# Kernel optimization log

Measured on AMD Instinct MI355X. Metric: run time of the kernel, lower is better.

The kernel has to match this reference:

```python
import jax, jax.numpy as jnp
import numpy as np


def _piecewise_weights(gt):
    # stats over gt[0,0]; torch.std uses ddof=1
    g00 = gt[0, 0]
    gmin = jnp.min(g00)
    gmean = jnp.mean(g00)
    gmax = jnp.max(g00)
    sd = jnp.std(g00, ddof=1)
    m1 = gmean + sd
    m2 = gmean + 3.0 * sd
    w_low = (gt - gmin) / (m1 - gmin) * 0.2
    w_mid = (gt - m1) / (m2 - m1) * 0.5 + 0.2
    w_high = (gt - m2) / (gmax - m2) * 0.3 + 0.7
    return jnp.where(gt <= m1, w_low, jnp.where(gt <= m2, w_mid, w_high))


def setup_inputs() -> dict:
    key = jax.random.key(0)
    k1, k2 = jax.random.split(key)
    shape = (1, 1, 4096, 4096)
    inputs = jax.random.normal(k1, shape, dtype=jnp.float32)
    targets = jax.random.normal(k2, shape, dtype=jnp.float32)
    return {"inputs": inputs, "targets": targets}


def reference(inputs, targets):
    # gt is a detached clone of targets -> no grad through the weights
    gt = jax.lax.stop_gradient(targets)
    weights = _piecewise_weights(gt)
    loss = jnp.abs(targets - inputs)
    return jnp.mean(loss * weights)
```

## Files before the change

kernel.cpp:

```cpp
#include <hip/hip_runtime.h>
#include <math.h>

#define BS 256
#define NBLK 1024
#define NWAVES (BS / 64)
#define NSLOT 64
#define PER_SLOT (NBLK / NSLOT)
#define FXS 4294967296.0


__device__ inline double wred_sum(double v) {
#pragma unroll
    for (int o = 32; o > 0; o >>= 1) v += __shfl_down(v, o, 64);
    return v;
}
__device__ inline float wred_min(float v) {
#pragma unroll
    for (int o = 32; o > 0; o >>= 1) v = fminf(v, __shfl_down(v, o, 64));
    return v;
}
__device__ inline float wred_max(float v) {
#pragma unroll
    for (int o = 32; o > 0; o >>= 1) v = fmaxf(v, __shfl_down(v, o, 64));
    return v;
}

__device__ inline void acc_stats(float4 v, double& s, double& ss, float& mn, float& mx) {
    mn = fminf(mn, fminf(fminf(v.x, v.y), fminf(v.z, v.w)));
    mx = fmaxf(mx, fmaxf(fmaxf(v.x, v.y), fmaxf(v.z, v.w)));
    s += (double)v.x + (double)v.y + (double)v.z + (double)v.w;
    ss += (double)v.x * v.x + (double)v.y * v.y
        + (double)v.z * v.z + (double)v.w * v.w;
}

__global__ void __launch_bounds__(BS) k_stats(
        const float* __restrict__ t, int n,
        double* __restrict__ bsum, double* __restrict__ bss,
        float* __restrict__ bmn, float* __restrict__ bmx,
        char* __restrict__ slots) {
    if (blockIdx.x == 0) {
        if (threadIdx.x < NSLOT)
            *(long long*)(slots + (size_t)threadIdx.x * 128) = 0ll;
        else if (threadIdx.x < 2 * NSLOT)
            *(unsigned*)(slots + 8192 + (size_t)(threadIdx.x - NSLOT) * 128) = 0u;
    }

    int tid = blockIdx.x * BS + threadIdx.x;
    const int stride = NBLK * BS;
    int n4 = n >> 2;
    const float4* t4 = (const float4*)t;

    double s = 0.0, ss = 0.0;
    float mn = 3.4e38f, mx = -3.4e38f;
    int i = tid;
    for (; i + 3 * stride < n4; i += 4 * stride) {
        float4 a = t4[i];
        float4 b = t4[i + stride];
        float4 c = t4[i + 2 * stride];
        float4 d = t4[i + 3 * stride];
        acc_stats(a, s, ss, mn, mx);
        acc_stats(b, s, ss, mn, mx);
        acc_stats(c, s, ss, mn, mx);
        acc_stats(d, s, ss, mn, mx);
    }
    for (; i < n4; i += stride) {
        float4 a = t4[i];
        acc_stats(a, s, ss, mn, mx);
    }
    if (tid == 0) {
        for (int j = (n4 << 2); j < n; j++) {
            float v = t[j];
            mn = fminf(mn, v); mx = fmaxf(mx, v);
            s += v; ss += (double)v * v;
        }
    }

    s = wred_sum(s); ss = wred_sum(ss); mn = wred_min(mn); mx = wred_max(mx);

    __shared__ double sh_s[NWAVES], sh_ss[NWAVES];
    __shared__ float sh_mn[NWAVES], sh_mx[NWAVES];
    int wid = threadIdx.x >> 6, lane = threadIdx.x & 63;
    if (lane == 0) { sh_s[wid] = s; sh_ss[wid] = ss; sh_mn[wid] = mn; sh_mx[wid] = mx; }
    __syncthreads();
    if (threadIdx.x == 0) {
        double S = sh_s[0], SS = sh_ss[0];
        float MN = sh_mn[0], MX = sh_mx[0];
        for (int k = 1; k < NWAVES; k++) {
            S += sh_s[k]; SS += sh_ss[k];
            MN = fminf(MN, sh_mn[k]); MX = fmaxf(MX, sh_mx[k]);
        }
        bsum[blockIdx.x] = S; bss[blockIdx.x] = SS;
        bmn[blockIdx.x] = MN; bmx[blockIdx.x] = MX;
    }
}

__device__ inline float welem(float g, float x, float gmin, float m1, float m2,
                              float sl, float sm, float shv) {
    float w = (g <= m1) ? (g - gmin) * sl
            : (g <= m2) ? (g - m1) * sm + 0.2f
                        : (g - m2) * shv + 0.7f;
    return fabsf(g - x) * w;
}

__global__ void __launch_bounds__(BS) k_loss(
        const float* __restrict__ x, const float* __restrict__ t, int n,
        const double* __restrict__ sbsum, const double* __restrict__ sbss,
        const float* __restrict__ sbmn, const float* __restrict__ sbmx,
        char* __restrict__ slots, float* __restrict__ out) {
    __shared__ double sh_s[NWAVES], sh_ss[NWAVES];
    __shared__ float sh_mn[NWAVES], sh_mx[NWAVES];
    __shared__ float s_c[8];
    {
        double s = 0.0, ss = 0.0;
        float mn = 3.4e38f, mx = -3.4e38f;
#pragma unroll 4
        for (int i = threadIdx.x; i < NBLK; i += BS) {
            s += sbsum[i]; ss += sbss[i];
            mn = fminf(mn, sbmn[i]); mx = fmaxf(mx, sbmx[i]);
        }
        s = wred_sum(s); ss = wred_sum(ss); mn = wred_min(mn); mx = wred_max(mx);
        int wid = threadIdx.x >> 6, lane = threadIdx.x & 63;
        if (lane == 0) { sh_s[wid] = s; sh_ss[wid] = ss; sh_mn[wid] = mn; sh_mx[wid] = mx; }
        __syncthreads();
        if (threadIdx.x == 0) {
            double S = sh_s[0], SS = sh_ss[0];
            float MN = sh_mn[0], MX = sh_mx[0];
            for (int k = 1; k < NWAVES; k++) {
                S += sh_s[k]; SS += sh_ss[k];
                MN = fminf(MN, sh_mn[k]); MX = fmaxf(MX, sh_mx[k]);
            }
            double dn = (double)n;
            double mean = S / dn;
            double var = (SS - S * S / dn) / (dn - 1.0);
            double sd = sqrt(var);
            float m1 = (float)(mean + sd);
            float m2 = (float)(mean + 3.0 * sd);
            s_c[0] = MN;
            s_c[1] = m1;
            s_c[2] = m2;
            s_c[3] = 0.2f / (m1 - MN);
            s_c[4] = 0.5f / (m2 - m1);
            s_c[5] = 0.3f / (MX - m2);
        }
        __syncthreads();
    }
    float gmin = s_c[0], m1 = s_c[1], m2 = s_c[2];
    float sl = s_c[3], sm = s_c[4], shv = s_c[5];

    int tid = blockIdx.x * BS + threadIdx.x;
    const int stride = NBLK * BS;
    int n4 = n >> 2;
    const float4* x4 = (const float4*)x;
    const float4* t4 = (const float4*)t;

    double acc = 0.0;
    int i = tid;
    for (; i + 3 * stride < n4; i += 4 * stride) {
        float4 t0 = t4[i];
        float4 t1 = t4[i + stride];
        float4 t2 = t4[i + 2 * stride];
        float4 t3 = t4[i + 3 * stride];
        float4 x0 = x4[i];
        float4 x1 = x4[i + stride];
        float4 x2 = x4[i + 2 * stride];
        float4 x3 = x4[i + 3 * stride];
        float e0 = welem(t0.x, x0.x, gmin, m1, m2, sl, sm, shv)
                 + welem(t0.y, x0.y, gmin, m1, m2, sl, sm, shv)
                 + welem(t0.z, x0.z, gmin, m1, m2, sl, sm, shv)
                 + welem(t0.w, x0.w, gmin, m1, m2, sl, sm, shv);
        float e1 = welem(t1.x, x1.x, gmin, m1, m2, sl, sm, shv)
                 + welem(t1.y, x1.y, gmin, m1, m2, sl, sm, shv)
                 + welem(t1.z, x1.z, gmin, m1, m2, sl, sm, shv)
                 + welem(t1.w, x1.w, gmin, m1, m2, sl, sm, shv);
        float e2 = welem(t2.x, x2.x, gmin, m1, m2, sl, sm, shv)
                 + welem(t2.y, x2.y, gmin, m1, m2, sl, sm, shv)
                 + welem(t2.z, x2.z, gmin, m1, m2, sl, sm, shv)
                 + welem(t2.w, x2.w, gmin, m1, m2, sl, sm, shv);
        float e3 = welem(t3.x, x3.x, gmin, m1, m2, sl, sm, shv)
                 + welem(t3.y, x3.y, gmin, m1, m2, sl, sm, shv)
                 + welem(t3.z, x3.z, gmin, m1, m2, sl, sm, shv)
                 + welem(t3.w, x3.w, gmin, m1, m2, sl, sm, shv);
        acc += (double)e0 + (double)e1 + (double)e2 + (double)e3;
    }
    for (; i < n4; i += stride) {
        float4 tv = t4[i], xv = x4[i];
        float e0 = welem(tv.x, xv.x, gmin, m1, m2, sl, sm, shv)
                 + welem(tv.y, xv.y, gmin, m1, m2, sl, sm, shv)
                 + welem(tv.z, xv.z, gmin, m1, m2, sl, sm, shv)
                 + welem(tv.w, xv.w, gmin, m1, m2, sl, sm, shv);
        acc += (double)e0;
    }
    if (tid == 0) {
        for (int j = (n4 << 2); j < n; j++)
            acc += (double)welem(t[j], x[j], gmin, m1, m2, sl, sm, shv);
    }

    acc = wred_sum(acc);
    __shared__ double sh_acc[NWAVES];
    __shared__ int s_fin;
    int wid = threadIdx.x >> 6, lane = threadIdx.x & 63;
    if (lane == 0) sh_acc[wid] = acc;
    __syncthreads();
    if (threadIdx.x == 0) {
        double S = sh_acc[0];
        for (int k = 1; k < NWAVES; k++) S += sh_acc[k];
        int slot = blockIdx.x & (NSLOT - 1);
        long long* lslot = (long long*)(slots + (size_t)slot * 128);
        unsigned*  cslot = (unsigned*)(slots + 8192 + (size_t)slot * 128);
        __hip_atomic_fetch_add(lslot, (long long)llrint(S * FXS),
                               __ATOMIC_RELAXED, __HIP_MEMORY_SCOPE_AGENT);
        asm volatile("s_waitcnt vmcnt(0)" ::: "memory");
        unsigned prev = __hip_atomic_fetch_add(cslot, 1u,
                               __ATOMIC_RELAXED, __HIP_MEMORY_SCOPE_AGENT);
        s_fin = (prev == PER_SLOT - 1) ? 1 : 0;
    }
    __syncthreads();
    if (!s_fin) return;

    if (threadIdx.x < 64) {
        unsigned total;
        do {
            unsigned c = __hip_atomic_load(
                (unsigned*)(slots + 8192 + (size_t)threadIdx.x * 128),
                __ATOMIC_RELAXED, __HIP_MEMORY_SCOPE_AGENT);
#pragma unroll
            for (int o = 32; o > 0; o >>= 1) c += __shfl_down(c, o, 64);
            total = __shfl(c, 0, 64);
            if (total != NBLK) __builtin_amdgcn_s_sleep(32);
        } while (total != NBLK);
        long long v = __hip_atomic_load(
            (long long*)(slots + (size_t)threadIdx.x * 128),
            __ATOMIC_RELAXED, __HIP_MEMORY_SCOPE_AGENT);
#pragma unroll
        for (int o = 32; o > 0; o >>= 1) v += __shfl_down(v, o, 64);
        if (threadIdx.x == 0)
            out[0] = (float)(((double)v / FXS) / (double)n);
    }
}

extern "C" void kernel_launch(void* const* d_in, const int* in_sizes, int n_in,
                              void* d_out, int out_size, void* d_ws, size_t ws_size,
                              hipStream_t stream) {
    const float* inp = (const float*)d_in[0];
    const float* tgt = (const float*)d_in[1];
    int n = in_sizes[0];

    char* ws = (char*)d_ws;
    double* bsum = (double*)(ws);
    double* bss  = (double*)(ws + 8192);
    float*  bmn  = (float*)(ws + 16384);
    float*  bmx  = (float*)(ws + 20480);
    char*   slots = ws + 24576;

    k_stats<<<NBLK, BS, 0, stream>>>(tgt, n, bsum, bss, bmn, bmx, slots);
    k_loss<<<NBLK, BS, 0, stream>>>(inp, tgt, n, bsum, bss, bmn, bmx,
                                    slots, (float*)d_out);
}
```

Baseline: 46.95 us.

## Switch to contiguous per-block chunks with 2048 blocks and branchless weight select

Doubles the grid to 2048 blocks and replaces the grid-stride loop with a contiguous chunk per block, so each block streams one local region of both tensors. The piecewise weight is now computed for all three branches with fma and then selected, which removes divergent branches, and the finalization and workspace layout are adjusted to the larger block count. The cost is more partial results and atomics to combine and a longer partial-stat reduction at the start of every loss block.

```diff
diff --git a/kernel.cpp b/kernel.cpp
--- a/kernel.cpp
+++ b/kernel.cpp
@@ -2,10 +2,10 @@
 #include <math.h>
 
 #define BS 256
-#define NBLK 1024
+#define NB 2048
 #define NWAVES (BS / 64)
 #define NSLOT 64
-#define PER_SLOT (NBLK / NSLOT)
+#define PER_SLOT (NB / NSLOT)
 #define FXS 4294967296.0
 
 
@@ -45,29 +45,30 @@
             *(unsigned*)(slots + 8192 + (size_t)(threadIdx.x - NSLOT) * 128) = 0u;
     }
 
-    int tid = blockIdx.x * BS + threadIdx.x;
-    const int stride = NBLK * BS;
     int n4 = n >> 2;
+    int cpb = (n4 + NB - 1) / NB;
+    int start = blockIdx.x * cpb;
+    int end = min(start + cpb, n4);
     const float4* t4 = (const float4*)t;
 
     double s = 0.0, ss = 0.0;
     float mn = 3.4e38f, mx = -3.4e38f;
-    int i = tid;
-    for (; i + 3 * stride < n4; i += 4 * stride) {
+    int i = start + threadIdx.x;
+    for (; i + 3 * BS < end; i += 4 * BS) {
         float4 a = t4[i];
-        float4 b = t4[i + stride];
-        float4 c = t4[i + 2 * stride];
-        float4 d = t4[i + 3 * stride];
+        float4 b = t4[i + BS];
+        float4 c = t4[i + 2 * BS];
+        float4 d = t4[i + 3 * BS];
         acc_stats(a, s, ss, mn, mx);
         acc_stats(b, s, ss, mn, mx);
         acc_stats(c, s, ss, mn, mx);
         acc_stats(d, s, ss, mn, mx);
     }
-    for (; i < n4; i += stride) {
+    for (; i < end; i += BS) {
         float4 a = t4[i];
         acc_stats(a, s, ss, mn, mx);
     }
-    if (tid == 0) {
+    if (blockIdx.x == 0 && threadIdx.x == 0) {
         for (int j = (n4 << 2); j < n; j++) {
             float v = t[j];
             mn = fminf(mn, v); mx = fmaxf(mx, v);
@@ -96,10 +97,20 @@
 
 __device__ inline float welem(float g, float x, float gmin, float m1, float m2,
                               float sl, float sm, float shv) {
-    float w = (g <= m1) ? (g - gmin) * sl
-            : (g <= m2) ? (g - m1) * sm + 0.2f
-                        : (g - m2) * shv + 0.7f;
-    return fabsf(g - x) * w;
+    float d = fabsf(g - x);
+    float wlo = (g - gmin) * sl;
+    float wmi = fmaf(g - m1, sm, 0.2f);
+    float whi = fmaf(g - m2, shv, 0.7f);
+    float w = (g <= m1) ? wlo : ((g <= m2) ? wmi : whi);
+    return d * w;
+}
+
+__device__ inline float wquad(float4 tv, float4 xv, float gmin, float m1,
+                              float m2, float sl, float sm, float shv) {
+    return welem(tv.x, xv.x, gmin, m1, m2, sl, sm, shv)
+         + welem(tv.y, xv.y, gmin, m1, m2, sl, sm, shv)
+         + welem(tv.z, xv.z, gmin, m1, m2, sl, sm, shv)
+         + welem(tv.w, xv.w, gmin, m1, m2, sl, sm, shv);
 }
 
 __global__ void __launch_bounds__(BS) k_loss(
@@ -113,8 +124,7 @@
     {
         double s = 0.0, ss = 0.0;
         float mn = 3.4e38f, mx = -3.4e38f;
-#pragma unroll 4
-        for (int i = threadIdx.x; i < NBLK; i += BS) {
+        for (int i = threadIdx.x; i < NB; i += BS) {
             s += sbsum[i]; ss += sbss[i];
             mn = fminf(mn, sbmn[i]); mx = fmaxf(mx, sbmx[i]);
         }
@@ -147,50 +157,35 @@
     float gmin = s_c[0], m1 = s_c[1], m2 = s_c[2];
     float sl = s_c[3], sm = s_c[4], shv = s_c[5];
 
-    int tid = blockIdx.x * BS + threadIdx.x;
-    const int stride = NBLK * BS;
     int n4 = n >> 2;
+    int cpb = (n4 + NB - 1) / NB;
+    int start = blockIdx.x * cpb;
+    int end = min(start + cpb, n4);
     const float4* x4 = (const float4*)x;
     const float4* t4 = (const float4*)t;
 
     double acc = 0.0;
-    int i = tid;
-    for (; i + 3 * stride < n4; i += 4 * stride) {
-        float4 t0 = t4[i];
-        float4 t1 = t4[i + stride];
-        float4 t2 = t4[i + 2 * stride];
-        float4 t3 = t4[i + 3 * stride];
-        float4 x0 = x4[i];
-        float4 x1 = x4[i + stride];
-        float4 x2 = x4[i + 2 * stride];
-        float4 x3 = x4[i + 3 * stride];
-        float e0 = welem(t0.x, x0.x, gmin, m1, m2, sl, sm, shv)
-                 + welem(t0.y, x0.y, gmin, m1, m2, sl, sm, shv)
-                 + welem(t0.z, x0.z, gmin, m1, m2, sl, sm, shv)
-                 + welem(t0.w, x0.w, gmin, m1, m2, sl, sm, shv);
-        float e1 = welem(t1.x, x1.x, gmin, m1, m2, sl, sm, shv)
-                 + welem(t1.y, x1.y, gmin, m1, m2, sl, sm, shv)
-                 + welem(t1.z, x1.z, gmin, m1, m2, sl, sm, shv)
-                 + welem(t1.w, x1.w, gmin, m1, m2, sl, sm, shv);
-        float e2 = welem(t2.x, x2.x, gmin, m1, m2, sl, sm, shv)
-                 + welem(t2.y, x2.y, gmin, m1, m2, sl, sm, shv)
-                 + welem(t2.z, x2.z, gmin, m1, m2, sl, sm, shv)
-                 + welem(t2.w, x2.w, gmin, m1, m2, sl, sm, shv);
-        float e3 = welem(t3.x, x3.x, gmin, m1, m2, sl, sm, shv)
-                 + welem(t3.y, x3.y, gmin, m1, m2, sl, sm, shv)
-                 + welem(t3.z, x3.z, gmin, m1, m2, sl, sm, shv)
-                 + welem(t3.w, x3.w, gmin, m1, m2, sl, sm, shv);
-        acc += (double)e0 + (double)e1 + (double)e2 + (double)e3;
-    }
-    for (; i < n4; i += stride) {
+    int i = start + threadIdx.x;
+    for (; i + 3 * BS < end; i += 4 * BS) {
+        float4 xa = x4[i];
+        float4 xb = x4[i + BS];
+        float4 xc = x4[i + 2 * BS];
+        float4 xd = x4[i + 3 * BS];
+        float4 ta = t4[i];
+        float4 tb = t4[i + BS];
+        float4 tc = t4[i + 2 * BS];
+        float4 td = t4[i + 3 * BS];
+        float e0 = wquad(ta, xa, gmin, m1, m2, sl, sm, shv);
+        float e1 = wquad(tb, xb, gmin, m1, m2, sl, sm, shv);
+        float e2 = wquad(tc, xc, gmin, m1, m2, sl, sm, shv);
+        float e3 = wquad(td, xd, gmin, m1, m2, sl, sm, shv);
+        acc += (double)(e0 + e1) + (double)(e2 + e3);
+    }
+    for (; i < end; i += BS) {
         float4 tv = t4[i], xv = x4[i];
-        float e0 = welem(tv.x, xv.x, gmin, m1, m2, sl, sm, shv)
-                 + welem(tv.y, xv.y, gmin, m1, m2, sl, sm, shv)
-                 + welem(tv.z, xv.z, gmin, m1, m2, sl, sm, shv)
-                 + welem(tv.w, xv.w, gmin, m1, m2, sl, sm, shv);
-        acc += (double)e0;
-    }
-    if (tid == 0) {
+        acc += (double)wquad(tv, xv, gmin, m1, m2, sl, sm, shv);
+    }
+    if (blockIdx.x == 0 && threadIdx.x == 0) {
         for (int j = (n4 << 2); j < n; j++)
             acc += (double)welem(t[j], x[j], gmin, m1, m2, sl, sm, shv);
     }
@@ -226,8 +221,8 @@
 #pragma unroll
             for (int o = 32; o > 0; o >>= 1) c += __shfl_down(c, o, 64);
             total = __shfl(c, 0, 64);
-            if (total != NBLK) __builtin_amdgcn_s_sleep(32);
-        } while (total != NBLK);
+            if (total != NB) __builtin_amdgcn_s_sleep(32);
+        } while (total != NB);
         long long v = __hip_atomic_load(
             (long long*)(slots + (size_t)threadIdx.x * 128),
             __ATOMIC_RELAXED, __HIP_MEMORY_SCOPE_AGENT);
@@ -246,13 +241,13 @@
     int n = in_sizes[0];
 
     char* ws = (char*)d_ws;
-    double* bsum = (double*)(ws);
-    double* bss  = (double*)(ws + 8192);
-    float*  bmn  = (float*)(ws + 16384);
-    float*  bmx  = (float*)(ws + 20480);
-    char*   slots = ws + 24576;
-
-    k_stats<<<NBLK, BS, 0, stream>>>(tgt, n, bsum, bss, bmn, bmx, slots);
-    k_loss<<<NBLK, BS, 0, stream>>>(inp, tgt, n, bsum, bss, bmn, bmx,
-                                    slots, (float*)d_out);
-}
+    double* sum1  = (double*)(ws);
+    double* ss1   = (double*)(ws + 16384);
+    float*  mn1   = (float*)(ws + 32768);
+    float*  mx1   = (float*)(ws + 40960);
+    char*   slots = ws + 49408;
+
+    k_stats<<<NB, BS, 0, stream>>>(tgt, n, sum1, ss1, mn1, mx1, slots);
+    k_loss<<<NB, BS, 0, stream>>>(inp, tgt, n, sum1, ss1, mn1, mx1,
+                                  slots, (float*)d_out);
+}
```

New measurement: 46.71 us. About the same (-0.5%).
